# Kernel optimization log

Hardware: AMD Instinct MI355X
Metric: run time of the kernel (lower is better)

The kernel has to match this reference:

```python
import jax, jax.numpy as jnp
import numpy as np

MIN = 1e-30
BLOCK = 64


def setup_inputs() -> dict:
    key = jax.random.key(0)
    ks = jax.random.split(key, 16)
    B, L, D, H, M, E, P, R = 4, 512, 768, 12, 48, 32, 512, 97
    inp = {
        "context": jax.random.normal(ks[0], (B, L, D), jnp.float32),
        "attention": jax.random.uniform(ks[1], (B, H, L, L), jnp.float32),
        "mention_map": jax.random.uniform(ks[2], (B, M, L), jnp.float32),
        "entity_map": jax.random.uniform(ks[3], (B, E, M), jnp.float32),
        "hts": jax.random.randint(ks[4], (B, P, 2), 0, E).astype(jnp.int64),
        "hW": jax.random.normal(ks[5], (D, D), jnp.float32) * 0.02,
        "hb": jnp.zeros((D,), jnp.float32),
        "tW": jax.random.normal(ks[6], (D, D), jnp.float32) * 0.02,
        "tb": jnp.zeros((D,), jnp.float32),
        "hcW": jax.random.normal(ks[7], (D, D), jnp.float32) * 0.02,
        "hcb": jnp.zeros((D,), jnp.float32),
        "tcW": jax.random.normal(ks[8], (D, D), jnp.float32) * 0.02,
        "tcb": jnp.zeros((D,), jnp.float32),
        "clasW": jax.random.normal(ks[9], (R, D * BLOCK), jnp.float32) * 0.02,
        "clasb": jnp.zeros((R,), jnp.float32),
    }
    return inp


def _group_bilinear(h, t, W, b):
    # h, t: [B, P, D]; grouped bilinear a la ATLOP: block-outer-product then linear
    B, P, D = h.shape
    nb = D // BLOCK
    h_ = h.reshape(B, P, nb, BLOCK)
    t_ = t.reshape(B, P, nb, BLOCK)
    feat = jnp.einsum("bpni,bpnj->bpnij", h_, t_).reshape(B, P, D * BLOCK)
    return feat @ W.T + b


def _forward(context, attention, mention_map, entity_map, hts,
             hW, hb, tW, tb, hcW, hcb, tcW, tcb, clasW, clasb):
    B = context.shape[0]
    bidx = jnp.arange(B)[:, None]
    h_idx = hts[..., 0]  # [B, P]
    t_idx = hts[..., 1]
    ht_mask = (hts.sum(-1) != 0)[..., None].astype(context.dtype)  # [B, P, 1]

    # ---- get_ht ----
    mention = mention_map @ context                       # [B, M, D]
    att_sum = attention.sum(axis=1)                       # [B, L, L]
    mention_att = mention_map @ att_sum @ jnp.swapaxes(mention_map, 1, 2)  # [B, M, M]
    entity_att = entity_map @ mention_att                 # [B, E, M]

    h_mask = entity_map[bidx, h_idx] * ht_mask            # [B, P, M]
    t_mask = entity_map[bidx, t_idx] * ht_mask
    h_att = entity_att[bidx, h_idx] * t_mask
    t_att = entity_att[bidx, t_idx] * h_mask
    h_att = h_att / (h_att.sum(-1, keepdims=True) + MIN)
    t_att = t_att / (t_att.sum(-1, keepdims=True) + MIN)
    h = (t_att @ mention) * ht_mask                       # [B, P, D]
    t = (h_att @ mention) * ht_mask

    # ---- context_pooling (entity_map projected to token space) ----
    em_tok = entity_map @ mention_map                     # [B, E, L]
    em_tok = em_tok / (em_tok.sum(-1, keepdims=True) + MIN)
    ent_att = jnp.einsum("bel,bhlm->bhem", em_tok, attention)  # [B, H, E, L]
    hA = ent_att[bidx, :, h_idx]                          # [B, P, H, L]
    tA = ent_att[bidx, :, t_idx]
    ctx_att = (hA * tA).sum(axis=2)                       # [B, P, L]
    ctx_att = ctx_att / (ctx_att.sum(-1, keepdims=True) + MIN)
    context_info = (ctx_att @ context) * ht_mask          # [B, P, D]

    h_info = context_info @ hcW.T + hcb
    t_info = context_info @ tcW.T + tcb
    h = jnp.tanh(h @ hW.T + hb + h_info)
    t = jnp.tanh(t @ tW.T + tb + t_info)
    return _group_bilinear(h, t, clasW, clasb)            # [B, P, R]


def reference(context, attention, mention_map, entity_map, hts,
              hW, hb, tW, tb, hcW, hcb, tcW, tcb, clasW, clasb):
    return _forward(context, attention, mention_map, entity_map, hts,
                    hW, hb, tW, tb, hcW, hcb, tcW, tcb, clasW, clasb)
```

## Files before the change

### kernel.cpp

```cpp
#include <hip/hip_runtime.h>
#include <math.h>

#define Bc 4
#define Lc 512
#define Dc 768
#define Hc 12
#define Mc 48
#define Ec 32
#define Pc 512
#define Rc 97
#define MINV 1e-30f
#define NSLICE 24

typedef _Float16 f16;
typedef __attribute__((ext_vector_type(8))) _Float16 f16x8;
typedef __attribute__((ext_vector_type(4))) _Float16 f16x4;
typedef __attribute__((ext_vector_type(16))) float f32x16;

__global__ __launch_bounds__(256) void k_prep(const float* __restrict__ hW, const float* __restrict__ tW,
                                              const float* __restrict__ hcW, const float* __restrict__ tcW,
                                              f16* __restrict__ hWb, f16* __restrict__ tWb,
                                              f16* __restrict__ hcWb, f16* __restrict__ tcWb,
                                              const float* __restrict__ clasW, f16* __restrict__ Wp,
                                              const float* __restrict__ ctx, f16* __restrict__ ctxT,
                                              const float* __restrict__ mm, f16* __restrict__ mmH,
                                              const float* __restrict__ em, f16* __restrict__ emtH) {
    __shared__ f16 Ts[64][72];
    __shared__ float rowS[Mc];
    __shared__ float red[256];
    __shared__ float inv;
    int bid = blockIdx.x;
    int tid = threadIdx.x;
    if (bid < 2048) {
        const int DD = Dc * Dc;
        int i = bid * 256 + tid;
        int stride = 2048 * 256;
        for (; i < 4 * DD; i += stride) {
            int sel = i / DD, j = i % DD;
            const float* s = (sel == 0) ? hW : (sel == 1) ? tW : (sel == 2) ? hcW : tcW;
            f16* d = (sel == 0) ? hWb : (sel == 1) ? tWb : (sel == 2) ? hcWb : tcWb;
            d[j] = (f16)s[j];
        }
    } else if (bid < 5120) {
        int gid = (bid - 2048) * 256 + tid;
        int lane = gid & 63; int f = gid >> 6;
        int rt = f & 3; int s = (f >> 2) & 3; int c = f >> 4;
        int n_l = lane & 31, kg = lane >> 5;
        int r = rt * 32 + n_l;
        f16x8 v;
        if (r < Rc) {
            const float* src = clasW + (size_t)r * (Dc * 64) + c * 64 + s * 16 + kg * 8;
#pragma unroll
            for (int j = 0; j < 8; ++j) v[j] = (f16)src[j];
        } else {
#pragma unroll
            for (int j = 0; j < 8; ++j) v[j] = (f16)0.f;
        }
        ((f16x8*)Wp)[gid] = v;
    } else if (bid < 5504) {
        int id = bid - 5120;
        int dt = id % 12; int lt = (id / 12) % 8; int b = id / 96;
        int l0 = lt * 64, d0 = dt * 64;
        int r = tid >> 2, cg = tid & 3;
        const float* src = ctx + ((size_t)b * Lc + l0 + r) * Dc + d0 + cg * 16;
#pragma unroll
        for (int u = 0; u < 4; ++u) {
            float4 v = ((const float4*)src)[u];
            Ts[cg * 16 + u * 4 + 0][r] = (f16)v.x;
            Ts[cg * 16 + u * 4 + 1][r] = (f16)v.y;
            Ts[cg * 16 + u * 4 + 2][r] = (f16)v.z;
            Ts[cg * 16 + u * 4 + 3][r] = (f16)v.w;
        }
        __syncthreads();
        int dr = tid >> 2, seg = tid & 3;
        f16* dst = ctxT + ((size_t)b * Dc + d0 + dr) * Lc + l0 + seg * 16;
        f16x8 o0, o1;
#pragma unroll
        for (int j = 0; j < 8; ++j) { o0[j] = Ts[dr][seg * 16 + j]; o1[j] = Ts[dr][seg * 16 + 8 + j]; }
        *(f16x8*)dst = o0;
        *(f16x8*)(dst + 8) = o1;
    } else if (bid < 5552) {
        int gid = (bid - 5504) * 256 + tid;
        const float4* src = (const float4*)(mm + (size_t)gid * 8);
        float4 v0 = src[0], v1 = src[1];
        f16x8 o;
        o[0] = (f16)v0.x; o[1] = (f16)v0.y; o[2] = (f16)v0.z; o[3] = (f16)v0.w;
        o[4] = (f16)v1.x; o[5] = (f16)v1.y; o[6] = (f16)v1.z; o[7] = (f16)v1.w;
        ((f16x8*)mmH)[gid] = o;
    } else {
        int be = bid - 5552; int b = be / Ec;
        if (tid < Mc) rowS[tid] = em[(size_t)be * Mc + tid];
        __syncthreads();
        float v0 = 0.f, v1 = 0.f;
        {
            const float* mb0 = mm + (size_t)b * Mc * Lc + tid;
            const float* mb1 = mm + (size_t)b * Mc * Lc + tid + 256;
            for (int m = 0; m < Mc; ++m) {
                v0 += rowS[m] * mb0[(size_t)m * Lc];
                v1 += rowS[m] * mb1[(size_t)m * Lc];
            }
        }
        red[tid] = v0 + v1;
        __syncthreads();
        for (int s = 128; s > 0; s >>= 1) { if (tid < s) red[tid] += red[tid + s]; __syncthreads(); }
        if (tid == 0) inv = 1.f / (red[0] + MINV);
        __syncthreads();
        emtH[(size_t)be * Lc + tid] = (f16)(v0 * inv);
        emtH[(size_t)be * Lc + tid + 256] = (f16)(v1 * inv);
    }
}

__global__ __launch_bounds__(256) void k_att_mention(const f16* __restrict__ mmH,
                                                     const f16* __restrict__ emtH,
                                                     const float* __restrict__ att,
                                                     float* __restrict__ tmpML,
                                                     float* __restrict__ eat,
                                                     const f16* __restrict__ ctxT,
                                                     float* __restrict__ mention) {
    __shared__ __align__(16) char smem[32768];
    int bid = blockIdx.x;
    int tid = threadIdx.x;
    int w = tid >> 6, lane = tid & 63;
    if (bid < 384) {
        f16* Ss   = (f16*)smem;
        f16* attS = (f16*)(smem + 12288);
        int mt = bid & 7; int bh = bid >> 3;
        int b = bh / Hc, h = bh % Hc;
        int m0 = mt * 64;
        int n_l = lane & 31, kg = lane >> 5;

        const float* ab = att + (size_t)bh * Lc * Lc + m0;
        int mRow = tid & 63, lg = tid >> 6;
        float pre[16];
#pragma unroll
        for (int q = 0; q < 16; ++q) pre[q] = ab[(size_t)(lg * 16 + q) * Lc + mRow];

        f32x16 acc[2];
#pragma unroll
        for (int nt = 0; nt < 2; ++nt)
#pragma unroll
            for (int i = 0; i < 16; ++i) acc[nt][i] = 0.f;

        for (int kc = 0; kc < 8; ++kc) {
            __syncthreads();
#pragma unroll
            for (int half = 0; half < 2; ++half) {
                int cc = lg * 2 + half;
                f16x8 v;
#pragma unroll
                for (int jj = 0; jj < 8; ++jj) v[jj] = (f16)pre[half * 8 + jj];
                ((f16x8*)attS)[mRow * 8 + (cc ^ (mRow & 7))] = v;
            }
#pragma unroll
            for (int k = 0; k < 3; ++k) {
                int idx = tid + k * 256;
                int row = idx >> 3, cc = idx & 7;
                f16x8 v;
                if (row < Mc) {
                    v = *(const f16x8*)(mmH + ((size_t)b * Mc + row) * Lc + kc * 64 + cc * 8);
                } else if (row < 80) {
                    v = *(const f16x8*)(emtH + ((size_t)b * Ec + row - Mc) * Lc + kc * 64 + cc * 8);
                } else {
#pragma unroll
                    for (int j = 0; j < 8; ++j) v[j] = (f16)0.f;
                }
                ((f16x8*)Ss)[row * 8 + (cc ^ (row & 7))] = v;
            }
            if (kc < 7) {
#pragma unroll
                for (int q = 0; q < 16; ++q)
                    pre[q] = ab[(size_t)((kc + 1) * 64 + lg * 16 + q) * Lc + mRow];
            }
            __syncthreads();
            if (w < 3) {
                int arow = w * 32 + n_l;
#pragma unroll
                for (int kk = 0; kk < 4; ++kk) {
                    int cc = kk * 2 + kg;
                    f16x8 a = ((const f16x8*)Ss)[arow * 8 + (cc ^ (arow & 7))];
#pragma unroll
                    for (int nt = 0; nt < 2; ++nt) {
                        int bcol = nt * 32 + n_l;
                        f16x8 bb = ((const f16x8*)attS)[bcol * 8 + (cc ^ (bcol & 7))];
                        acc[nt] = __builtin_amdgcn_mfma_f32_32x32x16_f16(a, bb, acc[nt], 0, 0, 0);
                    }
                }
            }
        }
        if (w < 3) {
#pragma unroll
            for (int nt = 0; nt < 2; ++nt)
#pragma unroll
                for (int reg = 0; reg < 16; ++reg) {
                    int row = (reg & 3) + 8 * (reg >> 2) + 4 * kg;
                    int rr = w * 32 + row;
                    int col = m0 + nt * 32 + n_l;
                    if (rr < Mc) {
                        atomicAdd(&tmpML[((size_t)b * Mc + rr) * Lc + col], acc[nt][reg]);
                    } else if (rr < 80) {
                        eat[(((size_t)b * Hc + h) * Ec + (rr - Mc)) * Lc + col] = acc[nt][reg];
                    }
                }
        }
    } else {
        f16* As = (f16*)smem;
        f16* Bs = (f16*)(smem + 16384);
        int id = bid - 384;
        int dt = id % 12; int b = id / 12;
        int d0 = dt * 64;
        int w_m = w & 1, w_n = w >> 1;
        int m_l = lane & 31, kg = lane >> 5;
        int r0 = tid >> 3, cc0 = tid & 7;
        int r1 = r0 + 32;
        int mr0 = (r0 < Mc) ? r0 : r0 - Mc;
        int mr1 = (r1 < Mc) ? r1 : r1 - Mc;
        f16x8 ar0, ar1, br0, br1;
        auto loadt = [&](int it) {
            int k0 = it * 64;
            ar0 = *(const f16x8*)(mmH + ((size_t)b * Mc + mr0) * Lc + k0 + cc0 * 8);
            ar1 = *(const f16x8*)(mmH + ((size_t)b * Mc + mr1) * Lc + k0 + cc0 * 8);
            br0 = *(const f16x8*)(ctxT + ((size_t)b * Dc + d0 + r0) * Lc + k0 + cc0 * 8);
            br1 = *(const f16x8*)(ctxT + ((size_t)b * Dc + d0 + r1) * Lc + k0 + cc0 * 8);
        };
        auto writet = [&](int p) {
            ((f16x8*)(As + p * 4096))[r0 * 8 + (cc0 ^ (r0 & 7))] = ar0;
            ((f16x8*)(As + p * 4096))[r1 * 8 + (cc0 ^ (r1 & 7))] = ar1;
            ((f16x8*)(Bs + p * 4096))[r0 * 8 + (cc0 ^ (r0 & 7))] = br0;
            ((f16x8*)(Bs + p * 4096))[r1 * 8 + (cc0 ^ (r1 & 7))] = br1;
        };
        loadt(0); writet(0); loadt(1);
        f32x16 acc;
#pragma unroll
        for (int i = 0; i < 16; ++i) acc[i] = 0.f;
        int ar = w_m * 32 + m_l;
        int br = w_n * 32 + m_l;
        for (int it = 0; it < 8; ++it) {
            int p = it & 1;
            __syncthreads();
            if (it < 7) writet(p ^ 1);
            if (it < 6) loadt(it + 2);
#pragma unroll
            for (int s = 0; s < 4; ++s) {
                int ck = s * 2 + kg;
                f16x8 a = ((const f16x8*)(As + p * 4096))[ar * 8 + (ck ^ (ar & 7))];
                f16x8 bv = ((const f16x8*)(Bs + p * 4096))[br * 8 + (ck ^ (br & 7))];
                acc = __builtin_amdgcn_mfma_f32_32x32x16_f16(a, bv, acc, 0, 0, 0);
            }
        }
#pragma unroll
        for (int reg = 0; reg < 16; ++reg) {
            int row = (reg & 3) + 8 * (reg >> 2) + 4 * kg;
            int m = w_m * 32 + row;
            if (m < Mc) mention[((size_t)b * Mc + m) * Dc + d0 + w_n * 32 + m_l] = acc[reg];
        }
    }
}

__global__ __launch_bounds__(256) void k_ma(const float* __restrict__ tmp,
                                            const float* __restrict__ mm,
                                            float* __restrict__ maS) {
    int wv = threadIdx.x >> 6, lane = threadIdx.x & 63;
    int gid = blockIdx.x * 4 + wv;
    int m2 = gid % 48;
    int m  = (gid / 48) % 48;
    int b  = gid / (48 * 48);
    const float4* t = (const float4*)(tmp + ((size_t)b * Mc + m)  * Lc);
    const float4* r = (const float4*)(mm  + ((size_t)b * Mc + m2) * Lc);
    float4 a0 = t[lane],      b0 = r[lane];
    float4 a1 = t[lane + 64], b1 = r[lane + 64];
    float acc = a0.x * b0.x + a0.y * b0.y + a0.z * b0.z + a0.w * b0.w
              + a1.x * b1.x + a1.y * b1.y + a1.z * b1.z + a1.w * b1.w;
#pragma unroll
    for (int off = 1; off < 64; off <<= 1) acc += __shfl_xor(acc, off);
    if (lane == 0) maS[gid] = acc;
}

__global__ __launch_bounds__(256) void k_ea(const float* __restrict__ maS,
                                            const float* __restrict__ em,
                                            float* __restrict__ ea) {
    __shared__ float S[48 * 48];
    int b  = blockIdx.x >> 3;
    int eg = blockIdx.x & 7;
    int tid = threadIdx.x;
    for (int i = tid; i < 48 * 48; i += 256) S[i] = maS[(size_t)b * 48 * 48 + i];
    __syncthreads();
    int wv = tid >> 6, lane = tid & 63;
    int e = eg * 4 + wv;
    if (lane < 48) {
        const float* emr = em + ((size_t)b * Ec + e) * Mc;
        float acc = 0.f;
#pragma unroll
        for (int m = 0; m < 48; ++m) acc += emr[m] * S[m * 48 + lane];
        ea[((size_t)b * Ec + e) * Mc + lane] = acc;
    }
}

__global__ __launch_bounds__(256) void k_pair(const int* __restrict__ hts,
                                              const float* __restrict__ em,
                                              const float* __restrict__ ea,
                                              const float* __restrict__ eat,
                                              f16* __restrict__ hatN, f16* __restrict__ tatN,
                                              f16* __restrict__ caH) {
    int wv = threadIdx.x >> 6, lane = threadIdx.x & 63;
    int bp = blockIdx.x * 4 + wv;
    int b = bp >> 9;
    int hi = hts[bp * 2], ti = hts[bp * 2 + 1];
    float mask = (hi + ti != 0) ? 1.f : 0.f;
    float hat = 0.f, tat = 0.f;
    if (lane < Mc) {
        float hm = em[((size_t)(b * Ec + hi)) * Mc + lane];
        float tm = em[((size_t)(b * Ec + ti)) * Mc + lane];
        float eh = ea[((size_t)(b * Ec + hi)) * Mc + lane];
        float et = ea[((size_t)(b * Ec + ti)) * Mc + lane];
        hat = eh * tm * mask;
        tat = et * hm * mask;
    }
    float sh = hat, st = tat;
#pragma unroll
    for (int off = 1; off < 64; off <<= 1) { sh += __shfl_xor(sh, off); st += __shfl_xor(st, off); }
    float hnorm = 1.f / (sh + MINV);
    float tnorm = 1.f / (st + MINV);
    hatN[(size_t)bp * 64 + lane] = (f16)(hat * hnorm);
    tatN[(size_t)bp * 64 + lane] = (f16)(tat * tnorm);

    const float* base = eat + (size_t)b * Hc * Ec * Lc;
    float prod[8];
    float tot = 0.f;
#pragma unroll
    for (int j8 = 0; j8 < 8; ++j8) {
        int j = j8 * 64 + lane;
        float a = 0.f;
#pragma unroll
        for (int h = 0; h < Hc; ++h)
            a += base[((size_t)h * Ec + hi) * Lc + j] * base[((size_t)h * Ec + ti) * Lc + j];
        prod[j8] = a;
        tot += a;
    }
#pragma unroll
    for (int off = 1; off < 64; off <<= 1) tot += __shfl_xor(tot, off);
    float inv = 1.f / (tot + MINV);
#pragma unroll
    for (int j8 = 0; j8 < 8; ++j8)
        caH[(size_t)bp * Lc + j8 * 64 + lane] = (f16)(prod[j8] * inv);
}

__global__ __launch_bounds__(256) void k_htci(const f16* __restrict__ tatN, const f16* __restrict__ hatN,
                                              const float* __restrict__ mention,
                                              f16* __restrict__ hB, f16* __restrict__ tB,
                                              const int* __restrict__ hts,
                                              const f16* __restrict__ caH,
                                              const f16* __restrict__ ctxT,
                                              f16* __restrict__ ci) {
    __shared__ __align__(16) char smem[33024];
    int bid = blockIdx.x;
    int tid = threadIdx.x;
    int w = tid >> 6, lane = tid & 63;
    int w_m = w & 1, w_n = w >> 1;
    int m_l = lane & 31, kg = lane >> 5;
    if (bid < 384) {
        f16* At = (f16*)smem;
        f16* Ah = (f16*)(smem + 8192);
        f16* Bs = (f16*)(smem + 16384);
        int m0 = (bid & 31) * 64;
        int b = m0 >> 9;
        int d0 = (bid >> 5) * 64;

        for (int i = tid; i < 512; i += 256) {
            int p = i >> 3, c = i & 7;
            ((f16x8*)At)[p * 8 + (c ^ (p & 7))] = *(const f16x8*)(tatN + (size_t)(m0 + p) * 64 + c * 8);
            ((f16x8*)Ah)[p * 8 + (c ^ (p & 7))] = *(const f16x8*)(hatN + (size_t)(m0 + p) * 64 + c * 8);
        }
        for (int i = tid; i < 512; i += 256) {
            f16x8 z;
#pragma unroll
            for (int j = 0; j < 8; ++j) z[j] = (f16)0.f;
            ((f16x8*)Bs)[i] = z;
        }
        __syncthreads();
        if (tid < 192) {
            int m = tid >> 2, q = tid & 3;
            const float4* src = (const float4*)(mention + ((size_t)b * Mc + m) * Dc + d0 + q * 16);
#pragma unroll
            for (int u = 0; u < 4; ++u) {
                float4 v = src[u];
                int dl = q * 16 + u * 4;
#pragma unroll
                for (int x = 0; x < 4; ++x) {
                    float vv = (x == 0) ? v.x : (x == 1) ? v.y : (x == 2) ? v.z : v.w;
                    int d = dl + x;
                    Bs[(d * 8 + ((m >> 3) ^ (d & 7))) * 8 + (m & 7)] = (f16)vv;
                }
            }
        }
        __syncthreads();

        f32x16 acch, acct;
#pragma unroll
        for (int i = 0; i < 16; ++i) { acch[i] = 0.f; acct[i] = 0.f; }
        int ar = w_m * 32 + m_l;
        int br = w_n * 32 + m_l;
#pragma unroll
        for (int s = 0; s < 4; ++s) {
            int ck = s * 2 + kg;
            f16x8 at_ = ((const f16x8*)At)[ar * 8 + (ck ^ (ar & 7))];
            f16x8 ah_ = ((const f16x8*)Ah)[ar * 8 + (ck ^ (ar & 7))];
            f16x8 bv = ((const f16x8*)Bs)[br * 8 + (ck ^ (br & 7))];
            acch = __builtin_amdgcn_mfma_f32_32x32x16_f16(at_, bv, acch, 0, 0, 0);
            acct = __builtin_amdgcn_mfma_f32_32x32x16_f16(ah_, bv, acct, 0, 0, 0);
        }
#pragma unroll
        for (int reg = 0; reg < 16; ++reg) {
            int row = (reg & 3) + 8 * (reg >> 2) + 4 * kg;
            int p = m0 + w_m * 32 + row;
            int d = d0 + w_n * 32 + m_l;
            hB[(size_t)p * Dc + d] = (f16)acch[reg];
            tB[(size_t)p * Dc + d] = (f16)acct[reg];
        }
    } else {
        f16* As = (f16*)smem;
        f16* Bs = (f16*)(smem + 16384);
        float* maskS = (float*)(smem + 32768);
        int id = bid - 384;
        int dt = id % 12; int pt = (id / 12) % 8; int b = id / 96;
        int p0 = pt * 64, d0 = dt * 64;
        int r0 = tid >> 3, cc0 = tid & 7;
        int r1 = r0 + 32;
        if (tid < 64) {
            int bp = b * Pc + p0 + tid;
            maskS[tid] = (hts[bp * 2] + hts[bp * 2 + 1] != 0) ? 1.f : 0.f;
        }
        f16x8 ar0, ar1, br0, br1;
        auto loadt = [&](int it) {
            int k0 = it * 64;
            ar0 = *(const f16x8*)(caH + (size_t)(b * Pc + p0 + r0) * Lc + k0 + cc0 * 8);
            ar1 = *(const f16x8*)(caH + (size_t)(b * Pc + p0 + r1) * Lc + k0 + cc0 * 8);
            br0 = *(const f16x8*)(ctxT + (size_t)(b * Dc + d0 + r0) * Lc + k0 + cc0 * 8);
            br1 = *(const f16x8*)(ctxT + (size_t)(b * Dc + d0 + r1) * Lc + k0 + cc0 * 8);
        };
        auto writet = [&](int p) {
            ((f16x8*)(As + p * 4096))[r0 * 8 + (cc0 ^ (r0 & 7))] = ar0;
            ((f16x8*)(As + p * 4096))[r1 * 8 + (cc0 ^ (r1 & 7))] = ar1;
            ((f16x8*)(Bs + p * 4096))[r0 * 8 + (cc0 ^ (r0 & 7))] = br0;
            ((f16x8*)(Bs + p * 4096))[r1 * 8 + (cc0 ^ (r1 & 7))] = br1;
        };
        loadt(0); writet(0); loadt(1);
        f32x16 acc;
#pragma unroll
        for (int i = 0; i < 16; ++i) acc[i] = 0.f;
        int ar = w_m * 32 + m_l;
        int br = w_n * 32 + m_l;
        for (int it = 0; it < 8; ++it) {
            int p = it & 1;
            __syncthreads();
            if (it < 7) writet(p ^ 1);
            if (it < 6) loadt(it + 2);
#pragma unroll
            for (int s = 0; s < 4; ++s) {
                int ck = s * 2 + kg;
                f16x8 a = ((const f16x8*)(As + p * 4096))[ar * 8 + (ck ^ (ar & 7))];
                f16x8 bv = ((const f16x8*)(Bs + p * 4096))[br * 8 + (ck ^ (br & 7))];
                acc = __builtin_amdgcn_mfma_f32_32x32x16_f16(a, bv, acc, 0, 0, 0);
            }
        }
#pragma unroll
        for (int reg = 0; reg < 16; ++reg) {
            int row = (reg & 3) + 8 * (reg >> 2) + 4 * kg;
            int p = p0 + w_m * 32 + row;
            int d = d0 + w_n * 32 + m_l;
            ci[(size_t)(b * Pc + p) * Dc + d] = (f16)(acc[reg] * maskS[w_m * 32 + row]);
        }
    }
}

__global__ __launch_bounds__(256) void k_proj_mfma(const f16* __restrict__ Xh, const f16* __restrict__ Wh,
                                                   const float* __restrict__ bh,
                                                   const f16* __restrict__ Xt, const f16* __restrict__ Wt,
                                                   const float* __restrict__ bt,
                                                   const f16* __restrict__ Xc, const f16* __restrict__ Whc,
                                                   const float* __restrict__ bhc,
                                                   const f16* __restrict__ Wtc, const float* __restrict__ btc,
                                                   f16* __restrict__ outh, f16* __restrict__ outt) {
    __shared__ __align__(16) f16 Xs[2][64 * 64];
    __shared__ __align__(16) f16 Ws[2][64 * 64];
    int z = blockIdx.z;
    const f16* X1 = z ? Xt : Xh;
    const f16* W1 = z ? Wt : Wh;
    const float* b1 = z ? bt : bh;
    const f16* W2 = z ? Wtc : Whc;
    const float* b2 = z ? btc : bhc;
    f16* outp = z ? outt : outh;
    int m0 = blockIdx.x * 64, n0 = blockIdx.y * 64;
    int tid = threadIdx.x;
    int w = tid >> 6, lane = tid & 63;
    int w_m = w & 1, w_n = w >> 1;
    int m_l = lane & 31, kg = lane >> 5;
    const f16* Xarr[2] = {X1, Xc};
    const f16* Warr[2] = {W1, W2};
    int r0 = tid >> 3, cc0 = tid & 7;
    int r1 = r0 + 32;
    f16x8 xr0, xr1, wr0, wr1;
    auto loadt = [&](int it) {
        int src = it / 12; int k0 = (it % 12) * 64;
        const f16* X = Xarr[src]; const f16* W = Warr[src];
        xr0 = *(const f16x8*)(X + (size_t)(m0 + r0) * Dc + k0 + cc0 * 8);
        xr1 = *(const f16x8*)(X + (size_t)(m0 + r1) * Dc + k0 + cc0 * 8);
        wr0 = *(const f16x8*)(W + (size_t)(n0 + r0) * Dc + k0 + cc0 * 8);
        wr1 = *(const f16x8*)(W + (size_t)(n0 + r1) * Dc + k0 + cc0 * 8);
    };
    auto writet = [&](int p) {
        ((f16x8*)Xs[p])[r0 * 8 + (cc0 ^ (r0 & 7))] = xr0;
        ((f16x8*)Xs[p])[r1 * 8 + (cc0 ^ (r1 & 7))] = xr1;
        ((f16x8*)Ws[p])[r0 * 8 + (cc0 ^ (r0 & 7))] = wr0;
        ((f16x8*)Ws[p])[r1 * 8 + (cc0 ^ (r1 & 7))] = wr1;
    };
    loadt(0); writet(0); loadt(1);
    f32x16 acc;
#pragma unroll
    for (int i = 0; i < 16; ++i) acc[i] = 0.f;
    int ar = w_m * 32 + m_l;
    int br = w_n * 32 + m_l;
    for (int it = 0; it < 24; ++it) {
        int p = it & 1;
        __syncthreads();
        if (it < 23) writet(p ^ 1);
        if (it < 22) loadt(it + 2);
#pragma unroll
        for (int s = 0; s < 4; ++s) {
            int ck = s * 2 + kg;
            f16x8 a = ((const f16x8*)Xs[p])[ar * 8 + (ck ^ (ar & 7))];
            f16x8 b = ((const f16x8*)Ws[p])[br * 8 + (ck ^ (br & 7))];
            acc = __builtin_amdgcn_mfma_f32_32x32x16_f16(a, b, acc, 0, 0, 0);
        }
    }
#pragma unroll
    for (int reg = 0; reg < 16; ++reg) {
        int row = (reg & 3) + 8 * (reg >> 2) + 4 * kg;
        int m = m0 + w_m * 32 + row;
        int n = n0 + w_n * 32 + m_l;
        float v = tanhf(acc[reg] + b1[n] + b2[n]);
        outp[(size_t)m * Dc + n] = (f16)v;
    }
}

__global__ __launch_bounds__(256, 3) void k_bilin(const f16* __restrict__ hF, const f16* __restrict__ tF,
                                                  const f16* __restrict__ Wp, f16* __restrict__ partial) {
    __shared__ __align__(16) f16 tS[128 * 64];
    __shared__ f16 hS[128 * 33];
    int id = blockIdx.x;
    int rh = id & 1;
    int st = id >> 1;
    int slice = st % NSLICE;
    int tile = st / NSLICE;
    int bp0 = tile * 128;
    int c0 = slice * 32;
    int n = c0 >> 6;
    int tid = threadIdx.x;
    int w = tid >> 6, lane = tid & 63;
    int w_m = w & 1, w_r = w >> 1;
    int m_l = lane & 31, kg = lane >> 5;
    int rt = rh * 2 + w_r;

    for (int idx = tid; idx < 128 * 4; idx += 256) {
        int bp = idx >> 2, seg = idx & 3;
        f16x8 hv = *(const f16x8*)(hF + (size_t)(bp0 + bp) * Dc + c0 + seg * 8);
#pragma unroll
        for (int j = 0; j < 8; ++j) hS[bp * 33 + seg * 8 + j] = hv[j];
    }
    for (int idx = tid; idx < 128 * 8; idx += 256) {
        int bp = idx >> 3, cc = idx & 7;
        f16x8 tv = *(const f16x8*)(tF + (size_t)(bp0 + bp) * Dc + n * 64 + cc * 8);
        ((f16x8*)tS)[bp * 8 + (cc ^ (bp & 7))] = tv;
    }
    __syncthreads();

    int rowA = w_m * 64 + m_l;
    int rowB = rowA + 32;

    f16x8 tvA[4], tvB[4];
#pragma unroll
    for (int s = 0; s < 4; ++s) {
        int ck = s * 2 + kg;
        tvA[s] = ((const f16x8*)tS)[rowA * 8 + (ck ^ (rowA & 7))];
        tvB[s] = ((const f16x8*)tS)[rowB * 8 + (ck ^ (rowB & 7))];
    }

    f32x16 acc[2];
#pragma unroll
    for (int mt = 0; mt < 2; ++mt)
#pragma unroll
        for (int i = 0; i < 16; ++i) acc[mt][i] = 0.f;

    const f16x8* wpb = (const f16x8*)Wp + ((size_t)c0 * 16 + rt) * 64 + lane;
    f16x8 BfA[4], BfB[4];
#pragma unroll
    for (int s = 0; s < 4; ++s) BfA[s] = wpb[s * 256];

    for (int io = 0; io < 32; io += 2) {
#pragma unroll
        for (int s = 0; s < 4; ++s) BfB[s] = wpb[(io + 1) * 1024 + s * 256];
        {
            f16 hv0 = hS[rowA * 33 + io];
            f16 hv1 = hS[rowB * 33 + io];
#pragma unroll
            for (int s = 0; s < 4; ++s) {
                f16x8 a0 = tvA[s] * hv0;
                f16x8 a1 = tvB[s] * hv1;
                acc[0] = __builtin_amdgcn_mfma_f32_32x32x16_f16(a0, BfA[s], acc[0], 0, 0, 0);
                acc[1] = __builtin_amdgcn_mfma_f32_32x32x16_f16(a1, BfA[s], acc[1], 0, 0, 0);
            }
        }
        if (io + 2 < 32) {
#pragma unroll
            for (int s = 0; s < 4; ++s) BfA[s] = wpb[(io + 2) * 1024 + s * 256];
        }
        {
            f16 hv0 = hS[rowA * 33 + io + 1];
            f16 hv1 = hS[rowB * 33 + io + 1];
#pragma unroll
            for (int s = 0; s < 4; ++s) {
                f16x8 a0 = tvA[s] * hv0;
                f16x8 a1 = tvB[s] * hv1;
                acc[0] = __builtin_amdgcn_mfma_f32_32x32x16_f16(a0, BfB[s], acc[0], 0, 0, 0);
                acc[1] = __builtin_amdgcn_mfma_f32_32x32x16_f16(a1, BfB[s], acc[1], 0, 0, 0);
            }
        }
    }

    f16* pbase = partial + (size_t)slice * (2048 * 128);
    int r = rt * 32 + m_l;
#pragma unroll
    for (int mt = 0; mt < 2; ++mt)
#pragma unroll
        for (int reg = 0; reg < 16; ++reg) {
            int row = (reg & 3) + 8 * (reg >> 2) + 4 * kg;
            int bp = bp0 + w_m * 64 + mt * 32 + row;
            pbase[(size_t)bp * 128 + r] = (f16)acc[mt][reg];
        }
}

__global__ __launch_bounds__(256) void k_reduce(const f16* __restrict__ partial,
                                                const float* __restrict__ cb,
                                                float* __restrict__ out) {
    int idx = blockIdx.x * 256 + threadIdx.x;
    int bp = idx >> 5, c = idx & 31;
    const f16x4* p = (const f16x4*)partial + idx;
    float a0 = 0.f, a1 = 0.f, a2 = 0.f, a3 = 0.f;
#pragma unroll
    for (int s = 0; s < NSLICE; ++s) {
        f16x4 v = p[(size_t)s * (2048 * 32)];
        a0 += (float)v[0]; a1 += (float)v[1]; a2 += (float)v[2]; a3 += (float)v[3];
    }
    int rb = c * 4;
    float* ob = out + (size_t)bp * Rc;
    if (rb + 0 < Rc) ob[rb + 0] = a0 + cb[rb + 0];
    if (rb + 1 < Rc) ob[rb + 1] = a1 + cb[rb + 1];
    if (rb + 2 < Rc) ob[rb + 2] = a2 + cb[rb + 2];
    if (rb + 3 < Rc) ob[rb + 3] = a3 + cb[rb + 3];
}

extern "C" void kernel_launch(void* const* d_in, const int* in_sizes, int n_in,
                              void* d_out, int out_size, void* d_ws, size_t ws_size,
                              hipStream_t stream) {
    const float* context   = (const float*)d_in[0];
    const float* attention = (const float*)d_in[1];
    const float* mm        = (const float*)d_in[2];
    const float* em        = (const float*)d_in[3];
    const int*   hts       = (const int*)d_in[4];
    const float* hW        = (const float*)d_in[5];
    const float* hb        = (const float*)d_in[6];
    const float* tW        = (const float*)d_in[7];
    const float* tb        = (const float*)d_in[8];
    const float* hcW       = (const float*)d_in[9];
    const float* hcb       = (const float*)d_in[10];
    const float* tcW       = (const float*)d_in[11];
    const float* tcb       = (const float*)d_in[12];
    const float* clasW     = (const float*)d_in[13];
    const float* clasb     = (const float*)d_in[14];
    float* out = (float*)d_out;

    char* wsb = (char*)d_ws;
    auto alloc = [&](size_t bytes) { char* p = wsb; wsb += (bytes + 255) & ~(size_t)255; return p; };
    float* mention     = (float*)alloc((size_t)Bc * Mc * Dc * 4);
    float* tmpML       = (float*)alloc((size_t)Bc * Mc * Lc * 4);
    float* entity_att  = (float*)alloc((size_t)Bc * Ec * Mc * 4);
    float* ent_att     = (float*)alloc((size_t)Bc * Hc * Ec * Lc * 4);
    float* maS         = (float*)alloc((size_t)Bc * Mc * Mc * 4);
    f16* em_tok  = (f16*)alloc((size_t)Bc * Ec * Lc * 2);
    f16* ctx_att = (f16*)alloc((size_t)Bc * Pc * Lc * 2);
    f16* mmH     = (f16*)alloc((size_t)Bc * Mc * Lc * 2);
    f16* hatN    = (f16*)alloc((size_t)Bc * Pc * 64 * 2);
    f16* tatN    = (f16*)alloc((size_t)Bc * Pc * 64 * 2);
    f16* h_buf   = (f16*)alloc((size_t)Bc * Pc * Dc * 2);
    f16* t_buf   = (f16*)alloc((size_t)Bc * Pc * Dc * 2);
    f16* ctxinfo = (f16*)alloc((size_t)Bc * Pc * Dc * 2);
    f16* h_fin   = (f16*)alloc((size_t)Bc * Pc * Dc * 2);
    f16* t_fin   = (f16*)alloc((size_t)Bc * Pc * Dc * 2);
    f16* hWb     = (f16*)alloc((size_t)Dc * Dc * 2);
    f16* tWb     = (f16*)alloc((size_t)Dc * Dc * 2);
    f16* hcWb    = (f16*)alloc((size_t)Dc * Dc * 2);
    f16* tcWb    = (f16*)alloc((size_t)Dc * Dc * 2);
    f16* ctxT    = (f16*)alloc((size_t)Bc * Dc * Lc * 2);
    f16* Wp      = (f16*)alloc((size_t)768 * 16 * 64 * 8 * 2);
    f16* partial = (f16*)alloc((size_t)NSLICE * 2048 * 128 * 2);

    hipMemsetAsync(tmpML, 0, (size_t)Bc * Mc * Lc * 4, stream);
    k_prep<<<dim3(5680), dim3(256), 0, stream>>>(hW, tW, hcW, tcW, hWb, tWb, hcWb, tcWb,
                                                 clasW, Wp, context, ctxT, mm, mmH, em, em_tok);
    k_att_mention<<<dim3(432), dim3(256), 0, stream>>>(mmH, em_tok, attention, tmpML, ent_att,
                                                       ctxT, mention);
    k_ma<<<dim3(Bc * Mc * Mc / 4), dim3(256), 0, stream>>>(tmpML, mm, maS);
    k_ea<<<dim3(Bc * 8), dim3(256), 0, stream>>>(maS, em, entity_att);
    k_pair<<<dim3(Bc * Pc / 4), dim3(256), 0, stream>>>(hts, em, entity_att, ent_att, hatN, tatN, ctx_att);
    k_htci<<<dim3(768), dim3(256), 0, stream>>>(tatN, hatN, mention, h_buf, t_buf,
                                                hts, ctx_att, ctxT, ctxinfo);
    k_proj_mfma<<<dim3(32, 12, 2), dim3(256), 0, stream>>>(h_buf, hWb, hb, t_buf, tWb, tb,
                                                           ctxinfo, hcWb, hcb, tcWb, tcb, h_fin, t_fin);
    k_bilin<<<dim3(16 * NSLICE * 2), dim3(256), 0, stream>>>(h_fin, t_fin, Wp, partial);
    k_reduce<<<dim3(256), dim3(256), 0, stream>>>(partial, clasb, out);
}
```

Before: 247.0 us.

## Fold memset and k_ea into other kernels; use direct global-to-LDS loads in projection

Zeroing of tmpML moves from a separate hipMemsetAsync into extra k_prep blocks. The k_ea kernel is removed and entity attention is computed inline in k_pair from maS and em. Weight casts in k_prep now use float4 loads. The projection GEMM stages tiles with global_load_lds instead of going through registers. The goal is fewer launches and less register-staging overhead, at the cost of redundant per-pair dot products in k_pair and a now single-stage prefetch pipeline in the GEMM.

```diff
diff --git a/kernel.cpp b/kernel.cpp
--- a/kernel.cpp
+++ b/kernel.cpp
@@ -24,7 +24,8 @@
                                               const float* __restrict__ clasW, f16* __restrict__ Wp,
                                               const float* __restrict__ ctx, f16* __restrict__ ctxT,
                                               const float* __restrict__ mm, f16* __restrict__ mmH,
-                                              const float* __restrict__ em, f16* __restrict__ emtH) {
+                                              const float* __restrict__ em, f16* __restrict__ emtH,
+                                              float* __restrict__ tmpML) {
     __shared__ f16 Ts[64][72];
     __shared__ float rowS[Mc];
     __shared__ float red[256];
@@ -32,14 +33,17 @@
     int bid = blockIdx.x;
     int tid = threadIdx.x;
     if (bid < 2048) {
-        const int DD = Dc * Dc;
+        const int Q = 147456;
         int i = bid * 256 + tid;
         int stride = 2048 * 256;
-        for (; i < 4 * DD; i += stride) {
-            int sel = i / DD, j = i % DD;
+        for (; i < 4 * Q; i += stride) {
+            int sel = i / Q, j = i % Q;
             const float* s = (sel == 0) ? hW : (sel == 1) ? tW : (sel == 2) ? hcW : tcW;
             f16* d = (sel == 0) ? hWb : (sel == 1) ? tWb : (sel == 2) ? hcWb : tcWb;
-            d[j] = (f16)s[j];
+            float4 v = ((const float4*)s)[j];
+            f16x4 o;
+            o[0] = (f16)v.x; o[1] = (f16)v.y; o[2] = (f16)v.z; o[3] = (f16)v.w;
+            ((f16x4*)d)[j] = o;
         }
     } else if (bid < 5120) {
         int gid = (bid - 2048) * 256 + tid;
@@ -87,7 +91,7 @@
         o[0] = (f16)v0.x; o[1] = (f16)v0.y; o[2] = (f16)v0.z; o[3] = (f16)v0.w;
         o[4] = (f16)v1.x; o[5] = (f16)v1.y; o[6] = (f16)v1.z; o[7] = (f16)v1.w;
         ((f16x8*)mmH)[gid] = o;
-    } else {
+    } else if (bid < 5680) {
         int be = bid - 5552; int b = be / Ec;
         if (tid < Mc) rowS[tid] = em[(size_t)be * Mc + tid];
         __syncthreads();
@@ -107,6 +111,12 @@
         __syncthreads();
         emtH[(size_t)be * Lc + tid] = (f16)(v0 * inv);
         emtH[(size_t)be * Lc + tid + 256] = (f16)(v1 * inv);
+    } else {
+        int base = ((bid - 5680) * 256 + tid) * 4;
+        float4 z = make_float4(0.f, 0.f, 0.f, 0.f);
+        float4* t4 = (float4*)tmpML;
+#pragma unroll
+        for (int u = 0; u < 4; ++u) t4[base + u] = z;
     }
 }
 
@@ -275,29 +285,9 @@
     if (lane == 0) maS[gid] = acc;
 }
 
-__global__ __launch_bounds__(256) void k_ea(const float* __restrict__ maS,
-                                            const float* __restrict__ em,
-                                            float* __restrict__ ea) {
-    __shared__ float S[48 * 48];
-    int b  = blockIdx.x >> 3;
-    int eg = blockIdx.x & 7;
-    int tid = threadIdx.x;
-    for (int i = tid; i < 48 * 48; i += 256) S[i] = maS[(size_t)b * 48 * 48 + i];
-    __syncthreads();
-    int wv = tid >> 6, lane = tid & 63;
-    int e = eg * 4 + wv;
-    if (lane < 48) {
-        const float* emr = em + ((size_t)b * Ec + e) * Mc;
-        float acc = 0.f;
-#pragma unroll
-        for (int m = 0; m < 48; ++m) acc += emr[m] * S[m * 48 + lane];
-        ea[((size_t)b * Ec + e) * Mc + lane] = acc;
-    }
-}
-
 __global__ __launch_bounds__(256) void k_pair(const int* __restrict__ hts,
                                               const float* __restrict__ em,
-                                              const float* __restrict__ ea,
+                                              const float* __restrict__ maS,
                                               const float* __restrict__ eat,
                                               f16* __restrict__ hatN, f16* __restrict__ tatN,
                                               f16* __restrict__ caH) {
@@ -310,8 +300,16 @@
     if (lane < Mc) {
         float hm = em[((size_t)(b * Ec + hi)) * Mc + lane];
         float tm = em[((size_t)(b * Ec + ti)) * Mc + lane];
-        float eh = ea[((size_t)(b * Ec + hi)) * Mc + lane];
-        float et = ea[((size_t)(b * Ec + ti)) * Mc + lane];
+        float eh = 0.f, et = 0.f;
+        const float* maB = maS + (size_t)b * Mc * Mc;
+        const float* emH = em + ((size_t)(b * Ec + hi)) * Mc;
+        const float* emT = em + ((size_t)(b * Ec + ti)) * Mc;
+#pragma unroll 8
+        for (int m = 0; m < Mc; ++m) {
+            float ms = maB[m * Mc + lane];
+            eh += emH[m] * ms;
+            et += emT[m] * ms;
+        }
         hat = eh * tm * mask;
         tat = et * hm * mask;
     }
@@ -496,24 +494,26 @@
     int m_l = lane & 31, kg = lane >> 5;
     const f16* Xarr[2] = {X1, Xc};
     const f16* Warr[2] = {W1, W2};
-    int r0 = tid >> 3, cc0 = tid & 7;
-    int r1 = r0 + 32;
-    f16x8 xr0, xr1, wr0, wr1;
-    auto loadt = [&](int it) {
+
+    auto stage = [&](int p, int it) {
         int src = it / 12; int k0 = (it % 12) * 64;
         const f16* X = Xarr[src]; const f16* W = Warr[src];
-        xr0 = *(const f16x8*)(X + (size_t)(m0 + r0) * Dc + k0 + cc0 * 8);
-        xr1 = *(const f16x8*)(X + (size_t)(m0 + r1) * Dc + k0 + cc0 * 8);
-        wr0 = *(const f16x8*)(W + (size_t)(n0 + r0) * Dc + k0 + cc0 * 8);
-        wr1 = *(const f16x8*)(W + (size_t)(n0 + r1) * Dc + k0 + cc0 * 8);
+#pragma unroll
+        for (int g = 0; g < 2; ++g) {
+            int s = g * 256 + w * 64 + lane;
+            int r = s >> 3, c = (s & 7) ^ (r & 7);
+            __builtin_amdgcn_global_load_lds(
+                (const __attribute__((address_space(1))) void*)(X + (size_t)(m0 + r) * Dc + k0 + c * 8),
+                (__attribute__((address_space(3))) void*)(&Xs[p][(g * 256 + w * 64) * 8]),
+                16, 0, 0);
+            __builtin_amdgcn_global_load_lds(
+                (const __attribute__((address_space(1))) void*)(W + (size_t)(n0 + r) * Dc + k0 + c * 8),
+                (__attribute__((address_space(3))) void*)(&Ws[p][(g * 256 + w * 64) * 8]),
+                16, 0, 0);
+        }
     };
-    auto writet = [&](int p) {
-        ((f16x8*)Xs[p])[r0 * 8 + (cc0 ^ (r0 & 7))] = xr0;
-        ((f16x8*)Xs[p])[r1 * 8 + (cc0 ^ (r1 & 7))] = xr1;
-        ((f16x8*)Ws[p])[r0 * 8 + (cc0 ^ (r0 & 7))] = wr0;
-        ((f16x8*)Ws[p])[r1 * 8 + (cc0 ^ (r1 & 7))] = wr1;
-    };
-    loadt(0); writet(0); loadt(1);
+
+    stage(0, 0);
     f32x16 acc;
 #pragma unroll
     for (int i = 0; i < 16; ++i) acc[i] = 0.f;
@@ -522,8 +522,7 @@
     for (int it = 0; it < 24; ++it) {
         int p = it & 1;
         __syncthreads();
-        if (it < 23) writet(p ^ 1);
-        if (it < 22) loadt(it + 2);
+        if (it < 23) stage(p ^ 1, it + 1);
 #pragma unroll
         for (int s = 0; s < 4; ++s) {
             int ck = s * 2 + kg;
@@ -682,7 +681,6 @@
     auto alloc = [&](size_t bytes) { char* p = wsb; wsb += (bytes + 255) & ~(size_t)255; return p; };
     float* mention     = (float*)alloc((size_t)Bc * Mc * Dc * 4);
     float* tmpML       = (float*)alloc((size_t)Bc * Mc * Lc * 4);
-    float* entity_att  = (float*)alloc((size_t)Bc * Ec * Mc * 4);
     float* ent_att     = (float*)alloc((size_t)Bc * Hc * Ec * Lc * 4);
     float* maS         = (float*)alloc((size_t)Bc * Mc * Mc * 4);
     f16* em_tok  = (f16*)alloc((size_t)Bc * Ec * Lc * 2);
@@ -703,14 +701,12 @@
     f16* Wp      = (f16*)alloc((size_t)768 * 16 * 64 * 8 * 2);
     f16* partial = (f16*)alloc((size_t)NSLICE * 2048 * 128 * 2);
 
-    hipMemsetAsync(tmpML, 0, (size_t)Bc * Mc * Lc * 4, stream);
-    k_prep<<<dim3(5680), dim3(256), 0, stream>>>(hW, tW, hcW, tcW, hWb, tWb, hcWb, tcWb,
-                                                 clasW, Wp, context, ctxT, mm, mmH, em, em_tok);
+    k_prep<<<dim3(5704), dim3(256), 0, stream>>>(hW, tW, hcW, tcW, hWb, tWb, hcWb, tcWb,
+                                                 clasW, Wp, context, ctxT, mm, mmH, em, em_tok, tmpML);
     k_att_mention<<<dim3(432), dim3(256), 0, stream>>>(mmH, em_tok, attention, tmpML, ent_att,
                                                        ctxT, mention);
     k_ma<<<dim3(Bc * Mc * Mc / 4), dim3(256), 0, stream>>>(tmpML, mm, maS);
-    k_ea<<<dim3(Bc * 8), dim3(256), 0, stream>>>(maS, em, entity_att);
-    k_pair<<<dim3(Bc * Pc / 4), dim3(256), 0, stream>>>(hts, em, entity_att, ent_att, hatN, tatN, ctx_att);
+    k_pair<<<dim3(Bc * Pc / 4), dim3(256), 0, stream>>>(hts, em, maS, ent_att, hatN, tatN, ctx_att);
     k_htci<<<dim3(768), dim3(256), 0, stream>>>(tatN, hatN, mention, h_buf, t_buf,
                                                 hts, ctx_att, ctxT, ctxinfo);
     k_proj_mfma<<<dim3(32, 12, 2), dim3(256), 0, stream>>>(h_buf, hWb, hb, t_buf, tWb, tb,
```

New measurement: 245.6 us. About the same (-0.6%).
